# Performance work log

Measured on AMD Instinct MI355X. Metric: run time of the kernel, lower is better.

The kernel has to match this reference:

```python
import jax, jax.numpy as jnp
import numpy as np

HIDDEN = 1024
NUM_HEADS = 16
HEAD_DIM = HIDDEN // NUM_HEADS
BLOCK_SIZE = 2048
LN_EPS = 1e-12


def layer_norm(x, g, b, eps=LN_EPS):
    mu = jnp.mean(x, axis=-1, keepdims=True)
    var = jnp.mean(jnp.square(x - mu), axis=-1, keepdims=True)
    return (x - mu) * jax.lax.rsqrt(var + eps) * g + b


def setup_inputs() -> dict:
    key = jax.random.key(0)
    ks = jax.random.split(key, 10)
    B, S_CTX, S_Q = 4, 8192, 2048
    scale = 1.0 / np.sqrt(HIDDEN)
    inp = {
        "input_ids": jax.random.normal(ks[0], (B, S_CTX, HIDDEN), jnp.float32),
        "query_input": jax.random.normal(ks[1], (B, S_Q, HIDDEN), jnp.float32),
        "Wq": jax.random.normal(ks[2], (HIDDEN, HIDDEN), jnp.float32) * scale,
        "bq": jnp.zeros((HIDDEN,), jnp.float32),
        "Wk": jax.random.normal(ks[3], (HIDDEN, HIDDEN), jnp.float32) * scale,
        "bk": jnp.zeros((HIDDEN,), jnp.float32),
        "Wv": jax.random.normal(ks[4], (HIDDEN, HIDDEN), jnp.float32) * scale,
        "bv": jnp.zeros((HIDDEN,), jnp.float32),
        "ln_g": jnp.ones((HIDDEN,), jnp.float32),
        "ln_b": jnp.zeros((HIDDEN,), jnp.float32),
        "host_id": 2,
    }
    return inp


def reference(input_ids, query_input, Wq, bq, Wk, bk, Wv, bv, ln_g, ln_b, host_id):
    B = input_ids.shape[0]
    start = host_id * BLOCK_SIZE  # host_id is a static Python int
    # Phase 1: local context encoding (anchor_key is computed in the original
    # but never used downstream, so it does not affect the output)
    local_block = input_ids[:, start:start + BLOCK_SIZE]          # (B, Skv, H)
    local_h = layer_norm(local_block, ln_g, ln_b)
    k = (local_h @ Wk + bk).reshape(B, BLOCK_SIZE, NUM_HEADS, HEAD_DIM)
    v = (local_h @ Wv + bv).reshape(B, BLOCK_SIZE, NUM_HEADS, HEAD_DIM)
    # Phase 2: query encoding; dropout is identity (p=0 / eval mode)
    Sq = query_input.shape[1]
    q_h = layer_norm(query_input, ln_g, ln_b)
    q = (q_h @ Wq + bq).reshape(B, Sq, NUM_HEADS, HEAD_DIM)
    scores = jnp.einsum("bqhd,bkhd->bhqk", q, k) / np.sqrt(HEAD_DIM)
    probs = jax.nn.softmax(scores, axis=-1)                       # (B, H, Sq, Skv)
    ctx = jnp.einsum("bhqk,bkhd->bqhd", probs, v)
    return ctx.reshape(B, Sq, HIDDEN)
```

## Files before the change

### kernel.cpp

```cpp
#include <hip/hip_runtime.h>

#define B_    4
#define SCTX  8192
#define SQ    2048
#define SK    2048
#define HID   1024
#define NH    16
#define HD    64
#define MQ    (B_*SQ)
#define MK    (B_*SK)

typedef float f32x4  __attribute__((ext_vector_type(4)));
typedef short bf16x8 __attribute__((ext_vector_type(8)));

__device__ __forceinline__ unsigned short f2b(float f) {
    union { float f; unsigned u; } v; v.f = f;
    unsigned r = v.u + 0x7FFFu + ((v.u >> 16) & 1u);
    return (unsigned short)(r >> 16);
}

__device__ __forceinline__ int decode_host_id(const unsigned* p) {
    unsigned w0 = p[0];
    int hid;
    if (w0 > 0u && w0 < 8u) hid = (int)w0;
    else if (w0 == 0u) {
        unsigned w1 = p[1];
        hid = (w1 == 0u) ? 0 : (int)__hiloint2double((int)w1, 0);
    } else hid = (int)__uint_as_float(w0);
    if (hid < 0) hid = 0;
    if (hid > SCTX/SK - 1) hid = SCTX/SK - 1;
    return hid;
}

__device__ __forceinline__ void gload16(const unsigned short* g, unsigned short* l) {
    __builtin_amdgcn_global_load_lds(
        (const __attribute__((address_space(1))) void*)g,
        (__attribute__((address_space(3))) void*)l, 16, 0, 0);
}

__global__ void ln_kernel(const float* __restrict__ query,
                          const float* __restrict__ input_ids,
                          const unsigned* __restrict__ host_id,
                          const float* __restrict__ g,
                          const float* __restrict__ lb,
                          unsigned short* __restrict__ hq,
                          unsigned short* __restrict__ hk) {
    int row = blockIdx.x;
    int start = decode_host_id(host_id) * SK;
    const float* src;
    unsigned short* dst;
    if (row < MQ) {
        src = query + (size_t)row * HID;
        dst = hq + (size_t)row * HID;
    } else {
        int r = row - MQ;
        int b = r >> 11, s = r & 2047;
        src = input_ids + ((size_t)b * SCTX + start + s) * HID;
        dst = hk + (size_t)r * HID;
    }
    int t = threadIdx.x;
    float4 x = ((const float4*)src)[t];
    float s1 = x.x + x.y + x.z + x.w;
    float s2 = x.x*x.x + x.y*x.y + x.z*x.z + x.w*x.w;
    for (int off = 32; off > 0; off >>= 1) {
        s1 += __shfl_xor(s1, off, 64);
        s2 += __shfl_xor(s2, off, 64);
    }
    __shared__ float red[8];
    int w = t >> 6;
    if ((t & 63) == 0) { red[w*2] = s1; red[w*2+1] = s2; }
    __syncthreads();
    s1 = red[0] + red[2] + red[4] + red[6];
    s2 = red[1] + red[3] + red[5] + red[7];
    float mu   = s1 * (1.0f / HID);
    float var  = s2 * (1.0f / HID) - mu * mu;
    float rstd = rsqrtf(fmaxf(var, 0.0f) + 1e-12f);
    float4 gv = ((const float4*)g)[t];
    float4 bv = ((const float4*)lb)[t];
    ushort4 o;
    o.x = f2b((x.x - mu) * rstd * gv.x + bv.x);
    o.y = f2b((x.y - mu) * rstd * gv.y + bv.y);
    o.z = f2b((x.z - mu) * rstd * gv.z + bv.z);
    o.w = f2b((x.w - mu) * rstd * gv.w + bv.w);
    ((ushort4*)dst)[t] = o;
}

__global__ void transpose_kernel(const float* __restrict__ src,
                                 unsigned short* __restrict__ dst) {
    __shared__ unsigned short tile[64][66];
    int tx = threadIdx.x & 63;
    int ty = threadIdx.x >> 6;
    int k0 = blockIdx.x * 64;
    int n0 = blockIdx.y * 64;
    for (int i = ty; i < 64; i += 4)
        tile[i][tx] = f2b(src[(size_t)(k0 + i) * HID + n0 + tx]);
    __syncthreads();
    for (int i = ty; i < 64; i += 4)
        dst[(size_t)(n0 + i) * HID + k0 + tx] = tile[tx][i];
}

#define BM 128
#define BN 128
#define BKg 32

__global__ __launch_bounds__(256, 3) void gemm3_kernel(
        const unsigned short* __restrict__ hq,
        const unsigned short* __restrict__ hk,
        const unsigned short* __restrict__ Wtq,
        const unsigned short* __restrict__ Wtk,
        const unsigned short* __restrict__ Wtv,
        const float* __restrict__ bq,
        const float* __restrict__ bk,
        const float* __restrict__ bv,
        unsigned short* __restrict__ Qb,
        unsigned short* __restrict__ Kb,
        unsigned short* __restrict__ Vtb) {
    __shared__ __align__(16) unsigned short As[BM * BKg];
    __shared__ __align__(16) unsigned short Bs[BN * BKg];

    int z = blockIdx.z;
    const unsigned short* A  = (z == 0) ? hq : hk;
    const unsigned short* Bt = (z == 0) ? Wtq : (z == 1) ? Wtk : Wtv;
    const float* bias        = (z == 0) ? bq  : (z == 1) ? bk  : bv;
    unsigned short* out      = (z == 0) ? Qb  : (z == 1) ? Kb  : Vtb;
    float scale = (z == 0) ? 0.125f : 1.0f;
    int epi = (z == 2);

    int t = threadIdx.x;
    int lane = t & 63;
    int w = t >> 6;
    int wr = w >> 1, wc = w & 1;
    int qd = lane >> 4, c = lane & 15;

    int bid = (int)(blockIdx.y * gridDim.x + blockIdx.x);
    int xcd = bid & 7, kk = bid >> 3;
    int bx = xcd * 8 + (kk & 7);
    int by = kk >> 3;
    size_t m0 = (size_t)bx * BM;
    size_t n0 = (size_t)by * BN;

    int s0 = t, s1 = t + 256;
    int ar0 = s0 >> 2, ac0 = (s0 & 3) * 8;
    int ar1 = s1 >> 2, ac1 = (s1 & 3) * 8;

    f32x4 acc[4][4] = {};
    for (int k0 = 0; k0 < HID; k0 += BKg) {
        __syncthreads();
        gload16(A  + (m0 + ar0) * HID + k0 + ac0, As + s0 * 8);
        gload16(A  + (m0 + ar1) * HID + k0 + ac1, As + s1 * 8);
        gload16(Bt + (n0 + ar0) * HID + k0 + ac0, Bs + s0 * 8);
        gload16(Bt + (n0 + ar1) * HID + k0 + ac1, Bs + s1 * 8);
        __syncthreads();
        bf16x8 a[4], b[4];
        #pragma unroll
        for (int mi = 0; mi < 4; mi++)
            a[mi] = *(const bf16x8*)(As + (wr*64 + mi*16 + c) * BKg + qd*8);
        #pragma unroll
        for (int ni = 0; ni < 4; ni++)
            b[ni] = *(const bf16x8*)(Bs + (wc*64 + ni*16 + c) * BKg + qd*8);
        #pragma unroll
        for (int mi = 0; mi < 4; mi++)
            #pragma unroll
            for (int ni = 0; ni < 4; ni++)
                acc[mi][ni] = __builtin_amdgcn_mfma_f32_16x16x32_bf16(a[mi], b[ni], acc[mi][ni], 0, 0, 0);
    }

    #pragma unroll
    for (int ni = 0; ni < 4; ni++) {
        int n = (int)n0 + wc*64 + ni*16 + c;
        float bn = bias[n];
        #pragma unroll
        for (int mi = 0; mi < 4; mi++) {
            int mbase = (int)m0 + wr*64 + mi*16 + qd*4;
            if (epi == 0) {
                #pragma unroll
                for (int r = 0; r < 4; r++)
                    out[(size_t)(mbase + r) * HID + n] = f2b((acc[mi][ni][r] + bn) * scale);
            } else {
                int bb = mbase >> 11, s = mbase & 2047;
                int h = n >> 6, d = n & 63;
                ushort4 pk;
                pk.x = f2b(acc[mi][ni][0] + bn);
                pk.y = f2b(acc[mi][ni][1] + bn);
                pk.z = f2b(acc[mi][ni][2] + bn);
                pk.w = f2b(acc[mi][ni][3] + bn);
                *(ushort4*)(out + (((size_t)(bb*NH + h))*HD + d)*SK + s) = pk;
            }
        }
    }
}

__global__ __launch_bounds__(64) void attn_kernel(
        const unsigned short* __restrict__ Q,
        const unsigned short* __restrict__ K,
        const unsigned short* __restrict__ Vt,
        float* __restrict__ out) {
    __shared__ __align__(16) unsigned short P[64][72];
    int lane = threadIdx.x;
    int qd = lane >> 4, c = lane & 15;
    int q0 = blockIdx.x * 64;
    int h  = blockIdx.y;
    int b  = blockIdx.z;

    bf16x8 qf[4][2];
    #pragma unroll
    for (int mi = 0; mi < 4; mi++)
        #pragma unroll
        for (int ks = 0; ks < 2; ks++)
            qf[mi][ks] = *(const bf16x8*)(Q + ((size_t)(b*SQ + q0 + mi*16 + c))*HID + h*HD + ks*32 + qd*8);

    float lsum[4][4];
    f32x4 o[4][4] = {};
    #pragma unroll
    for (int mi = 0; mi < 4; mi++)
        #pragma unroll
        for (int r = 0; r < 4; r++) lsum[mi][r] = 0.0f;

    for (int kt = 0; kt < SK/64; kt++) {
        int key0 = kt * 64;
        bf16x8 kf[4][2];
        #pragma unroll
        for (int ni = 0; ni < 4; ni++)
            #pragma unroll
            for (int ks = 0; ks < 2; ks++)
                kf[ni][ks] = *(const bf16x8*)(K + ((size_t)(b*SK + key0 + ni*16 + c))*HID + h*HD + ks*32 + qd*8);
        f32x4 s[4][4] = {};
        #pragma unroll
        for (int mi = 0; mi < 4; mi++)
            #pragma unroll
            for (int ni = 0; ni < 4; ni++) {
                s[mi][ni] = __builtin_amdgcn_mfma_f32_16x16x32_bf16(qf[mi][0], kf[ni][0], s[mi][ni], 0, 0, 0);
                s[mi][ni] = __builtin_amdgcn_mfma_f32_16x16x32_bf16(qf[mi][1], kf[ni][1], s[mi][ni], 0, 0, 0);
            }
        bf16x8 vf[4][2];
        #pragma unroll
        for (int ni = 0; ni < 4; ni++)
            #pragma unroll
            for (int ks = 0; ks < 2; ks++)
                vf[ni][ks] = *(const bf16x8*)(Vt + (((size_t)(b*NH + h))*HD + ni*16 + c)*SK + key0 + ks*32 + qd*8);
        #pragma unroll
        for (int mi = 0; mi < 4; mi++) {
            #pragma unroll
            for (int ni = 0; ni < 4; ni++)
                #pragma unroll
                for (int r = 0; r < 4; r++) {
                    float p = __expf(fminf(s[mi][ni][r], 40.0f));
                    s[mi][ni][r] = p;
                    lsum[mi][r] += p;
                }
            #pragma unroll
            for (int ni = 0; ni < 4; ni++)
                #pragma unroll
                for (int r = 0; r < 4; r++)
                    P[mi*16 + qd*4 + r][ni*16 + c] = f2b(s[mi][ni][r]);
        }
        asm volatile("s_waitcnt lgkmcnt(0)" ::: "memory");
        bf16x8 pf[4][2];
        #pragma unroll
        for (int mi = 0; mi < 4; mi++)
            #pragma unroll
            for (int ks = 0; ks < 2; ks++)
                pf[mi][ks] = *(const bf16x8*)(&P[mi*16 + c][ks*32 + qd*8]);
        #pragma unroll
        for (int mi = 0; mi < 4; mi++)
            #pragma unroll
            for (int ni = 0; ni < 4; ni++) {
                o[mi][ni] = __builtin_amdgcn_mfma_f32_16x16x32_bf16(pf[mi][0], vf[ni][0], o[mi][ni], 0, 0, 0);
                o[mi][ni] = __builtin_amdgcn_mfma_f32_16x16x32_bf16(pf[mi][1], vf[ni][1], o[mi][ni], 0, 0, 0);
            }
    }
    #pragma unroll
    for (int mi = 0; mi < 4; mi++)
        #pragma unroll
        for (int r = 0; r < 4; r++) {
            float l = lsum[mi][r];
            for (int off = 1; off < 16; off <<= 1) l += __shfl_xor(l, off, 16);
            lsum[mi][r] = 1.0f / l;
        }
    #pragma unroll
    for (int mi = 0; mi < 4; mi++)
        #pragma unroll
        for (int ni = 0; ni < 4; ni++)
            #pragma unroll
            for (int r = 0; r < 4; r++) {
                int m = q0 + mi*16 + qd*4 + r;
                out[((size_t)(b*SQ + m))*HID + h*HD + ni*16 + c] = o[mi][ni][r] * lsum[mi][r];
            }
}

extern "C" void kernel_launch(void* const* d_in, const int* in_sizes, int n_in,
                              void* d_out, int out_size, void* d_ws, size_t ws_size,
                              hipStream_t stream) {
    const float *input_ids = nullptr, *query = nullptr;
    const float *Ws[3] = {nullptr, nullptr, nullptr};
    const float *bs[5] = {nullptr, nullptr, nullptr, nullptr, nullptr};
    const unsigned *hostid = nullptr;
    int wi = 0, bi = 0;
    for (int i = 0; i < n_in; i++) {
        long sz = in_sizes[i];
        if      (sz == 33554432) input_ids = (const float*)d_in[i];
        else if (sz == 8388608)  query     = (const float*)d_in[i];
        else if (sz == 1048576)  { if (wi < 3) Ws[wi++] = (const float*)d_in[i]; }
        else if (sz == 1024)     { if (bi < 5) bs[bi++] = (const float*)d_in[i]; }
        else if (sz == 1 || sz == 2) hostid = (const unsigned*)d_in[i];
    }
    if (n_in != 11 || !input_ids || !query || wi != 3 || bi != 5 || !hostid) {
        input_ids = (const float*)d_in[0];  query = (const float*)d_in[1];
        Ws[0] = (const float*)d_in[2]; bs[0] = (const float*)d_in[3];
        Ws[1] = (const float*)d_in[4]; bs[1] = (const float*)d_in[5];
        Ws[2] = (const float*)d_in[6]; bs[2] = (const float*)d_in[7];
        bs[3] = (const float*)d_in[8]; bs[4] = (const float*)d_in[9];
        hostid = (const unsigned*)d_in[10];
    }
    const float *Wq = Ws[0], *Wk = Ws[1], *Wv = Ws[2];
    const float *bq = bs[0], *bk = bs[1], *bv = bs[2], *ln_g = bs[3], *ln_b = bs[4];
    float* out = (float*)d_out;

    char* ws = (char*)d_ws;
    unsigned short* hq  = (unsigned short*)ws; ws += (size_t)MQ * HID * 2;
    unsigned short* hk  = (unsigned short*)ws; ws += (size_t)MK * HID * 2;
    unsigned short* Wtq = (unsigned short*)ws; ws += (size_t)HID * HID * 2;
    unsigned short* Wtk = (unsigned short*)ws; ws += (size_t)HID * HID * 2;
    unsigned short* Wtv = (unsigned short*)ws; ws += (size_t)HID * HID * 2;
    unsigned short* Qb  = (unsigned short*)ws; ws += (size_t)MQ * HID * 2;
    unsigned short* Kb  = (unsigned short*)ws; ws += (size_t)MK * HID * 2;
    unsigned short* Vtb = (unsigned short*)ws; ws += (size_t)MK * HID * 2;

    ln_kernel<<<MQ + MK, 256, 0, stream>>>(query, input_ids, hostid, ln_g, ln_b, hq, hk);
    transpose_kernel<<<dim3(16, 16), 256, 0, stream>>>(Wq, Wtq);
    transpose_kernel<<<dim3(16, 16), 256, 0, stream>>>(Wk, Wtk);
    transpose_kernel<<<dim3(16, 16), 256, 0, stream>>>(Wv, Wtv);
    gemm3_kernel<<<dim3(MQ/BM, HID/BN, 3), 256, 0, stream>>>(
        hq, hk, Wtq, Wtk, Wtv, bq, bk, bv, Qb, Kb, Vtb);
    attn_kernel<<<dim3(SQ/64, NH, B_), 64, 0, stream>>>(Qb, Kb, Vtb, out);
}
```

Measured before the change: 435.3 us.

## Transpose attention MFMA operands so scores and output are key/dim-major per lane

Swaps the MFMA operand order in both attention matmuls so each lane holds a column of query positions. The softmax row sum then reduces with two cross-lane shuffles instead of per-row 16-lane reductions. P is written to shared memory as packed 8-byte stores using hardware bf16 pack conversion, and the output is stored as 16-byte vectors. The log2(e) factor is folded into the Q scale so exp2f replaces __expf. It keeps the unnormalized exponent with a clamp, as before, and trades the wider stores for a changed register layout and different LDS bank access patterns.

```diff
diff --git a/kernel.cpp b/kernel.cpp
--- a/kernel.cpp
+++ b/kernel.cpp
@@ -123,7 +123,7 @@
     const unsigned short* Bt = (z == 0) ? Wtq : (z == 1) ? Wtk : Wtv;
     const float* bias        = (z == 0) ? bq  : (z == 1) ? bk  : bv;
     unsigned short* out      = (z == 0) ? Qb  : (z == 1) ? Kb  : Vtb;
-    float scale = (z == 0) ? 0.125f : 1.0f;
+    float scale = (z == 0) ? 0.18033688f : 1.0f;
     int epi = (z == 2);
 
     int t = threadIdx.x;
@@ -204,88 +204,85 @@
 
     bf16x8 qf[4][2];
     #pragma unroll
-    for (int mi = 0; mi < 4; mi++)
+    for (int qi = 0; qi < 4; qi++)
         #pragma unroll
         for (int ks = 0; ks < 2; ks++)
-            qf[mi][ks] = *(const bf16x8*)(Q + ((size_t)(b*SQ + q0 + mi*16 + c))*HID + h*HD + ks*32 + qd*8);
-
-    float lsum[4][4];
+            qf[qi][ks] = *(const bf16x8*)(Q + ((size_t)(b*SQ + q0 + qi*16 + c))*HID + h*HD + ks*32 + qd*8);
+
+    float lsum[4] = {0.0f, 0.0f, 0.0f, 0.0f};
     f32x4 o[4][4] = {};
-    #pragma unroll
-    for (int mi = 0; mi < 4; mi++)
-        #pragma unroll
-        for (int r = 0; r < 4; r++) lsum[mi][r] = 0.0f;
 
     for (int kt = 0; kt < SK/64; kt++) {
         int key0 = kt * 64;
         bf16x8 kf[4][2];
         #pragma unroll
-        for (int ni = 0; ni < 4; ni++)
+        for (int si = 0; si < 4; si++)
             #pragma unroll
             for (int ks = 0; ks < 2; ks++)
-                kf[ni][ks] = *(const bf16x8*)(K + ((size_t)(b*SK + key0 + ni*16 + c))*HID + h*HD + ks*32 + qd*8);
-        f32x4 s[4][4] = {};
-        #pragma unroll
-        for (int mi = 0; mi < 4; mi++)
-            #pragma unroll
-            for (int ni = 0; ni < 4; ni++) {
-                s[mi][ni] = __builtin_amdgcn_mfma_f32_16x16x32_bf16(qf[mi][0], kf[ni][0], s[mi][ni], 0, 0, 0);
-                s[mi][ni] = __builtin_amdgcn_mfma_f32_16x16x32_bf16(qf[mi][1], kf[ni][1], s[mi][ni], 0, 0, 0);
+                kf[si][ks] = *(const bf16x8*)(K + ((size_t)(b*SK + key0 + si*16 + c))*HID + h*HD + ks*32 + qd*8);
+        f32x4 st[4][4] = {};
+        #pragma unroll
+        for (int si = 0; si < 4; si++)
+            #pragma unroll
+            for (int qi = 0; qi < 4; qi++) {
+                st[si][qi] = __builtin_amdgcn_mfma_f32_16x16x32_bf16(kf[si][0], qf[qi][0], st[si][qi], 0, 0, 0);
+                st[si][qi] = __builtin_amdgcn_mfma_f32_16x16x32_bf16(kf[si][1], qf[qi][1], st[si][qi], 0, 0, 0);
             }
         bf16x8 vf[4][2];
         #pragma unroll
-        for (int ni = 0; ni < 4; ni++)
+        for (int si = 0; si < 4; si++)
             #pragma unroll
             for (int ks = 0; ks < 2; ks++)
-                vf[ni][ks] = *(const bf16x8*)(Vt + (((size_t)(b*NH + h))*HD + ni*16 + c)*SK + key0 + ks*32 + qd*8);
-        #pragma unroll
-        for (int mi = 0; mi < 4; mi++) {
-            #pragma unroll
-            for (int ni = 0; ni < 4; ni++)
+                vf[si][ks] = *(const bf16x8*)(Vt + (((size_t)(b*NH + h))*HD + si*16 + c)*SK + key0 + ks*32 + qd*8);
+        #pragma unroll
+        for (int qi = 0; qi < 4; qi++)
+            #pragma unroll
+            for (int si = 0; si < 4; si++)
                 #pragma unroll
                 for (int r = 0; r < 4; r++) {
-                    float p = __expf(fminf(s[mi][ni][r], 40.0f));
-                    s[mi][ni][r] = p;
-                    lsum[mi][r] += p;
+                    float p = exp2f(fminf(st[si][qi][r], 50.0f));
+                    st[si][qi][r] = p;
+                    lsum[qi] += p;
                 }
-            #pragma unroll
-            for (int ni = 0; ni < 4; ni++)
-                #pragma unroll
-                for (int r = 0; r < 4; r++)
-                    P[mi*16 + qd*4 + r][ni*16 + c] = f2b(s[mi][ni][r]);
-        }
+        #pragma unroll
+        for (int qi = 0; qi < 4; qi++)
+            #pragma unroll
+            for (int si = 0; si < 4; si++) {
+                unsigned w0, w1;
+                asm("v_cvt_pk_bf16_f32 %0, %1, %2" : "=v"(w0) : "v"(st[si][qi][0]), "v"(st[si][qi][1]));
+                asm("v_cvt_pk_bf16_f32 %0, %1, %2" : "=v"(w1) : "v"(st[si][qi][2]), "v"(st[si][qi][3]));
+                uint2 pk; pk.x = w0; pk.y = w1;
+                *(uint2*)(&P[qi*16 + c][si*16 + qd*4]) = pk;
+            }
         asm volatile("s_waitcnt lgkmcnt(0)" ::: "memory");
         bf16x8 pf[4][2];
         #pragma unroll
-        for (int mi = 0; mi < 4; mi++)
+        for (int qi = 0; qi < 4; qi++)
             #pragma unroll
             for (int ks = 0; ks < 2; ks++)
-                pf[mi][ks] = *(const bf16x8*)(&P[mi*16 + c][ks*32 + qd*8]);
-        #pragma unroll
-        for (int mi = 0; mi < 4; mi++)
-            #pragma unroll
-            for (int ni = 0; ni < 4; ni++) {
-                o[mi][ni] = __builtin_amdgcn_mfma_f32_16x16x32_bf16(pf[mi][0], vf[ni][0], o[mi][ni], 0, 0, 0);
-                o[mi][ni] = __builtin_amdgcn_mfma_f32_16x16x32_bf16(pf[mi][1], vf[ni][1], o[mi][ni], 0, 0, 0);
+                pf[qi][ks] = *(const bf16x8*)(&P[qi*16 + c][ks*32 + qd*8]);
+        #pragma unroll
+        for (int si = 0; si < 4; si++)
+            #pragma unroll
+            for (int qi = 0; qi < 4; qi++) {
+                o[si][qi] = __builtin_amdgcn_mfma_f32_16x16x32_bf16(vf[si][0], pf[qi][0], o[si][qi], 0, 0, 0);
+                o[si][qi] = __builtin_amdgcn_mfma_f32_16x16x32_bf16(vf[si][1], pf[qi][1], o[si][qi], 0, 0, 0);
             }
     }
     #pragma unroll
-    for (int mi = 0; mi < 4; mi++)
-        #pragma unroll
-        for (int r = 0; r < 4; r++) {
-            float l = lsum[mi][r];
-            for (int off = 1; off < 16; off <<= 1) l += __shfl_xor(l, off, 16);
-            lsum[mi][r] = 1.0f / l;
+    for (int qi = 0; qi < 4; qi++) {
+        float l = lsum[qi];
+        l += __shfl_xor(l, 16, 64);
+        l += __shfl_xor(l, 32, 64);
+        lsum[qi] = 1.0f / l;
+    }
+    #pragma unroll
+    for (int si = 0; si < 4; si++)
+        #pragma unroll
+        for (int qi = 0; qi < 4; qi++) {
+            f32x4 ov = o[si][qi] * lsum[qi];
+            *(f32x4*)(out + ((size_t)(b*SQ + q0 + qi*16 + c))*HID + h*HD + si*16 + qd*4) = ov;
         }
-    #pragma unroll
-    for (int mi = 0; mi < 4; mi++)
-        #pragma unroll
-        for (int ni = 0; ni < 4; ni++)
-            #pragma unroll
-            for (int r = 0; r < 4; r++) {
-                int m = q0 + mi*16 + qd*4 + r;
-                out[((size_t)(b*SQ + m))*HID + h*HD + ni*16 + c] = o[mi][ni][r] * lsum[mi][r];
-            }
 }
 
 extern "C" void kernel_launch(void* const* d_in, const int* in_sizes, int n_in,
```

Measured after the change: 473.7 us. 1.09x slower.

## Double-buffer GEMM LDS tiles, fold log2e into Q scale, merge weight transposes

Applied to the files above, without the earlier changes.

The projection GEMM now uses two LDS buffers, so the next K-tile's global loads are issued before the current tile's MFMAs. This cuts the loop to one barrier per iteration instead of two. The Q scale now includes log2(e), so the attention softmax can use exp2f in place of __expf, with the clamp threshold adjusted to match. The three weight-transpose launches are merged into one launch over a z dimension. Doubling the GEMM's LDS footprint may lower occupancy under the launch bounds.

```diff
diff --git a/kernel.cpp b/kernel.cpp
--- a/kernel.cpp
+++ b/kernel.cpp
@@ -85,9 +85,16 @@
     ((ushort4*)dst)[t] = o;
 }
 
-__global__ void transpose_kernel(const float* __restrict__ src,
-                                 unsigned short* __restrict__ dst) {
+__global__ void transpose_kernel(const float* __restrict__ Wq,
+                                 const float* __restrict__ Wk,
+                                 const float* __restrict__ Wv,
+                                 unsigned short* __restrict__ Wtq,
+                                 unsigned short* __restrict__ Wtk,
+                                 unsigned short* __restrict__ Wtv) {
     __shared__ unsigned short tile[64][66];
+    int z = blockIdx.z;
+    const float* src = (z == 0) ? Wq : (z == 1) ? Wk : Wv;
+    unsigned short* dst = (z == 0) ? Wtq : (z == 1) ? Wtk : Wtv;
     int tx = threadIdx.x & 63;
     int ty = threadIdx.x >> 6;
     int k0 = blockIdx.x * 64;
@@ -115,15 +122,15 @@
         unsigned short* __restrict__ Qb,
         unsigned short* __restrict__ Kb,
         unsigned short* __restrict__ Vtb) {
-    __shared__ __align__(16) unsigned short As[BM * BKg];
-    __shared__ __align__(16) unsigned short Bs[BN * BKg];
+    __shared__ __align__(16) unsigned short As[2][BM * BKg];
+    __shared__ __align__(16) unsigned short Bs[2][BN * BKg];
 
     int z = blockIdx.z;
     const unsigned short* A  = (z == 0) ? hq : hk;
     const unsigned short* Bt = (z == 0) ? Wtq : (z == 1) ? Wtk : Wtv;
     const float* bias        = (z == 0) ? bq  : (z == 1) ? bk  : bv;
     unsigned short* out      = (z == 0) ? Qb  : (z == 1) ? Kb  : Vtb;
-    float scale = (z == 0) ? 0.125f : 1.0f;
+    float scale = (z == 0) ? 0.18033688f : 1.0f;
     int epi = (z == 2);
 
     int t = threadIdx.x;
@@ -143,27 +150,36 @@
     int ar0 = s0 >> 2, ac0 = (s0 & 3) * 8;
     int ar1 = s1 >> 2, ac1 = (s1 & 3) * 8;
 
+#define STAGE(buf, kk0) do { \
+    gload16(A  + (m0 + ar0) * HID + (kk0) + ac0, &As[buf][s0 * 8]); \
+    gload16(A  + (m0 + ar1) * HID + (kk0) + ac1, &As[buf][s1 * 8]); \
+    gload16(Bt + (n0 + ar0) * HID + (kk0) + ac0, &Bs[buf][s0 * 8]); \
+    gload16(Bt + (n0 + ar1) * HID + (kk0) + ac1, &Bs[buf][s1 * 8]); \
+} while (0)
+
     f32x4 acc[4][4] = {};
-    for (int k0 = 0; k0 < HID; k0 += BKg) {
-        __syncthreads();
-        gload16(A  + (m0 + ar0) * HID + k0 + ac0, As + s0 * 8);
-        gload16(A  + (m0 + ar1) * HID + k0 + ac1, As + s1 * 8);
-        gload16(Bt + (n0 + ar0) * HID + k0 + ac0, Bs + s0 * 8);
-        gload16(Bt + (n0 + ar1) * HID + k0 + ac1, Bs + s1 * 8);
-        __syncthreads();
+    STAGE(0, 0);
+    __syncthreads();
+    int cur = 0;
+    #pragma unroll 2
+    for (int kt = 0; kt < HID/BKg; kt++) {
+        if (kt + 1 < HID/BKg) STAGE(cur ^ 1, (kt + 1) * BKg);
         bf16x8 a[4], b[4];
         #pragma unroll
         for (int mi = 0; mi < 4; mi++)
-            a[mi] = *(const bf16x8*)(As + (wr*64 + mi*16 + c) * BKg + qd*8);
+            a[mi] = *(const bf16x8*)(&As[cur][(wr*64 + mi*16 + c) * BKg + qd*8]);
         #pragma unroll
         for (int ni = 0; ni < 4; ni++)
-            b[ni] = *(const bf16x8*)(Bs + (wc*64 + ni*16 + c) * BKg + qd*8);
+            b[ni] = *(const bf16x8*)(&Bs[cur][(wc*64 + ni*16 + c) * BKg + qd*8]);
         #pragma unroll
         for (int mi = 0; mi < 4; mi++)
             #pragma unroll
             for (int ni = 0; ni < 4; ni++)
                 acc[mi][ni] = __builtin_amdgcn_mfma_f32_16x16x32_bf16(a[mi], b[ni], acc[mi][ni], 0, 0, 0);
-    }
+        __syncthreads();
+        cur ^= 1;
+    }
+#undef STAGE
 
     #pragma unroll
     for (int ni = 0; ni < 4; ni++) {
@@ -244,7 +260,7 @@
             for (int ni = 0; ni < 4; ni++)
                 #pragma unroll
                 for (int r = 0; r < 4; r++) {
-                    float p = __expf(fminf(s[mi][ni][r], 40.0f));
+                    float p = exp2f(fminf(s[mi][ni][r], 50.0f));
                     s[mi][ni][r] = p;
                     lsum[mi][r] += p;
                 }
@@ -327,9 +343,7 @@
     unsigned short* Vtb = (unsigned short*)ws; ws += (size_t)MK * HID * 2;
 
     ln_kernel<<<MQ + MK, 256, 0, stream>>>(query, input_ids, hostid, ln_g, ln_b, hq, hk);
-    transpose_kernel<<<dim3(16, 16), 256, 0, stream>>>(Wq, Wtq);
-    transpose_kernel<<<dim3(16, 16), 256, 0, stream>>>(Wk, Wtk);
-    transpose_kernel<<<dim3(16, 16), 256, 0, stream>>>(Wv, Wtv);
+    transpose_kernel<<<dim3(16, 16, 3), 256, 0, stream>>>(Wq, Wk, Wv, Wtq, Wtk, Wtv);
     gemm3_kernel<<<dim3(MQ/BM, HID/BN, 3), 256, 0, stream>>>(
         hq, hk, Wtq, Wtk, Wtv, bq, bk, bv, Qb, Kb, Vtb);
     attn_kernel<<<dim3(SQ/64, NH, B_), 64, 0, stream>>>(Qb, Kb, Vtb, out);
```

Result: no change. 443.5 us (+1.9%).
